# Kernel optimization log

Measured on AMD Instinct MI355X. Metric: run time of the kernel, lower is better.

## Reference

```python
import jax, jax.numpy as jnp
import numpy as np

B = 32; H = 56; W = 56; DIM = 384; HEADS = 12; WIN = 7; SHIFT = 3
HEAD_DIM = DIM // HEADS; SCALE = HEAD_DIM ** -0.5
N = WIN * WIN; NW = (H // WIN) * (W // WIN); L = H * W + 1; HID = 4 * DIM


def _rel_index():
    coords = np.stack(np.meshgrid(np.arange(WIN), np.arange(WIN), indexing='ij')).reshape(2, -1)
    rel = (coords[:, :, None] - coords[:, None, :]).transpose(1, 2, 0)
    rel[:, :, 0] += WIN - 1
    rel[:, :, 1] += WIN - 1
    rel[:, :, 0] *= 2 * WIN - 1
    return jnp.asarray(rel.sum(-1))  # (N, N) int


def _attn_mask():
    # standard Swin shift mask, padded with a zero column so the cls key is always visible
    img = np.zeros((H, W))
    sl = (slice(0, -WIN), slice(-WIN, -SHIFT), slice(-SHIFT, None))
    cnt = 0
    for hs in sl:
        for ws in sl:
            img[hs, ws] = cnt
            cnt += 1
    mw = img.reshape(H // WIN, WIN, W // WIN, WIN).transpose(0, 2, 1, 3).reshape(-1, N)
    m = mw[:, None, :] - mw[:, :, None]
    m = np.where(m != 0, -100.0, 0.0).astype(np.float32)
    m = np.pad(m, ((0, 0), (0, 0), (1, 0)))  # (nW, N, N+1)
    return jnp.asarray(m)


REL_INDEX = _rel_index()
ATTN_MASK = _attn_mask()


def _ln(x, g, b, eps=1e-5):
    m = x.mean(-1, keepdims=True)
    v = ((x - m) ** 2).mean(-1, keepdims=True)
    return (x - m) * jax.lax.rsqrt(v + eps) * g + b


def setup_inputs() -> dict:
    key = jax.random.key(0)
    ks = jax.random.split(key, 6)
    s = 0.02
    return dict(
        x=jax.random.normal(ks[0], (B, L, DIM), jnp.float32),
        norm1_g=jnp.ones((DIM,), jnp.float32), norm1_b=jnp.zeros((DIM,), jnp.float32),
        qkv_w=jax.random.normal(ks[1], (3 * DIM, DIM), jnp.float32) * s,
        qkv_b=jnp.zeros((3 * DIM,), jnp.float32),
        rel_bias_table=jax.random.normal(ks[2], ((2 * WIN - 1) ** 2, HEADS), jnp.float32) * s,
        proj_w=jax.random.normal(ks[3], (DIM, DIM), jnp.float32) * s,
        proj_b=jnp.zeros((DIM,), jnp.float32),
        norm2_g=jnp.ones((DIM,), jnp.float32), norm2_b=jnp.zeros((DIM,), jnp.float32),
        fc1_w=jax.random.normal(ks[4], (HID, DIM), jnp.float32) * s,
        fc1_b=jnp.zeros((HID,), jnp.float32),
        fc2_w=jax.random.normal(ks[5], (DIM, HID), jnp.float32) * s,
        fc2_b=jnp.zeros((DIM,), jnp.float32),
    )


def reference(x, norm1_g, norm1_b, qkv_w, qkv_b, rel_bias_table, proj_w, proj_b,
              norm2_g, norm2_b, fc1_w, fc1_b, fc2_w, fc2_b):
    Bx = x.shape[0]
    shortcut = x
    h = _ln(x, norm1_g, norm1_b)
    qkv = h @ qkv_w.T + qkv_b  # (B, L, 3C)

    # ---- global cls attention: token 0 attends to every token (ClsAttention) ----
    t = qkv.reshape(Bx, L, 3, HEADS, HEAD_DIM).transpose(2, 0, 3, 1, 4)  # (3, B, h, L, d)
    q0 = t[0, :, :, 0:1, :] * SCALE
    cls_attn = jax.nn.softmax(jnp.einsum('bhqd,bhkd->bhqk', q0, t[1]), axis=-1)
    cls_out = jnp.einsum('bhqk,bhkd->bhqd', cls_attn, t[2]).transpose(0, 2, 1, 3).reshape(Bx, 1, DIM)

    # ---- shifted-window attention for patch tokens, cls qkv prepended per window ----
    cls_qkv = qkv[:, :1]  # (B, 1, 3C)
    p = qkv[:, 1:].reshape(Bx, H, W, 3 * DIM)
    p = jnp.roll(p, (-SHIFT, -SHIFT), axis=(1, 2))
    pw = p.reshape(Bx, H // WIN, WIN, W // WIN, WIN, 3 * DIM).transpose(0, 1, 3, 2, 4, 5)
    pw = pw.reshape(Bx * NW, N, 3 * DIM)
    cls_rep = jnp.broadcast_to(cls_qkv[:, None], (Bx, NW, 1, 3 * DIM)).reshape(Bx * NW, 1, 3 * DIM)
    qkvw = jnp.concatenate([cls_rep, pw], axis=1)  # (B*nW, N+1, 3C)

    tw = qkvw.reshape(Bx * NW, N + 1, 3, HEADS, HEAD_DIM).transpose(2, 0, 3, 1, 4)
    q = tw[0, :, :, 1:, :] * SCALE  # patch queries (B*nW, h, N, d)
    attn = jnp.einsum('bhqd,bhkd->bhqk', q, tw[1])  # (B*nW, h, N, N+1)
    rel = rel_bias_table[REL_INDEX.reshape(-1)].reshape(N, N, HEADS).transpose(2, 0, 1)
    attn = jnp.concatenate([attn[..., :1], attn[..., 1:] + rel[None]], axis=-1)
    attn = attn.reshape(Bx, NW, HEADS, N, N + 1) + ATTN_MASK[None, :, None]
    attn = jax.nn.softmax(attn.reshape(Bx * NW, HEADS, N, N + 1), axis=-1)
    xw = jnp.einsum('bhqk,bhkd->bhqd', attn, tw[2]).transpose(0, 2, 1, 3).reshape(Bx * NW, N, DIM)

    # window reverse + reverse cyclic shift
    xp = xw.reshape(Bx, H // WIN, W // WIN, WIN, WIN, DIM).transpose(0, 1, 3, 2, 4, 5).reshape(Bx, H, W, DIM)
    xp = jnp.roll(xp, (SHIFT, SHIFT), axis=(1, 2)).reshape(Bx, H * W, DIM)

    a = jnp.concatenate([cls_out, xp], axis=1) @ proj_w.T + proj_b
    x1 = shortcut + a
    h2 = _ln(x1, norm2_g, norm2_b)
    h2 = jax.nn.gelu(h2 @ fc1_w.T + fc1_b, approximate=False)
    return x1 + (h2 @ fc2_w.T + fc2_b)
```

## Files before the change

### kernel.cpp

```cpp
#include <hip/hip_runtime.h>

#define DEVI __device__ __forceinline__

typedef __attribute__((ext_vector_type(8))) __bf16 bf16x8;
typedef __attribute__((ext_vector_type(4))) float f32x4;
typedef unsigned short u16;
typedef unsigned int u32;

static constexpr int kB = 32;
static constexpr int kL = 3137;
static constexpr int kM = kB * kL;
static constexpr int kHeads = 12;
static constexpr float kScale = 0.17677669529663687f;
static constexpr int kNC = 13;

DEVI u16 f2b(float f) {
  u32 u = __float_as_uint(f);
  u32 r = (u + 0x7fffu + ((u >> 16) & 1u)) >> 16;
  return (u16)r;
}
DEVI float blo(u32 u) { return __uint_as_float(u << 16); }
DEVI float bhi(u32 u) { return __uint_as_float(u & 0xffff0000u); }
DEVI float b2f(u16 h) { return __uint_as_float(((u32)h) << 16); }

DEVI void async16(const void* g, void* l) {
  __builtin_amdgcn_global_load_lds((const __attribute__((address_space(1))) u32*)g,
                                   (__attribute__((address_space(3))) u32*)l, 16, 0, 0);
}

DEVI float wred_max(float v) {
#pragma unroll
  for (int o = 32; o; o >>= 1) v = fmaxf(v, __shfl_xor(v, o));
  return v;
}
DEVI float wred_sum(float v) {
#pragma unroll
  for (int o = 32; o; o >>= 1) v += __shfl_xor(v, o);
  return v;
}

__global__ void cvt_bf16(const float* __restrict__ in, u16* __restrict__ out, int n) {
  int i = blockIdx.x * 256 + threadIdx.x;
  if (i < n) out[i] = f2b(in[i]);
}

__global__ __launch_bounds__(64)
void ln384(const float* __restrict__ x, const float* __restrict__ g,
           const float* __restrict__ b, u16* __restrict__ out, int rows) {
  int row = blockIdx.x;
  if (row >= rows) return;
  const float* xr = x + (size_t)row * 384;
  int t = threadIdx.x;
  float v[6], s = 0.f, s2 = 0.f;
#pragma unroll
  for (int i = 0; i < 6; i++) {
    v[i] = xr[t + 64 * i];
    s += v[i];
    s2 += v[i] * v[i];
  }
  s = wred_sum(s);
  s2 = wred_sum(s2);
  float mean = s * (1.f / 384.f);
  float var = s2 * (1.f / 384.f) - mean * mean;
  float rinv = rsqrtf(var + 1e-5f);
  u16* orow = out + (size_t)row * 384;
#pragma unroll
  for (int i = 0; i < 6; i++) {
    int c = t + 64 * i;
    orow[c] = f2b((v[i] - mean) * rinv * g[c] + b[c]);
  }
}

DEVI float gelu_exact(float v) { return 0.5f * v * (1.f + erff(v * 0.70710678118654752f)); }

template <int EPI>
__global__ __launch_bounds__(256)
void gemm_bt(const u16* __restrict__ A, const u16* __restrict__ W,
             const float* __restrict__ bias, const float* __restrict__ res,
             void* __restrict__ outp, int M, int N, int K, int NX) {
  {
  }
  const int nwg = gridDim.x;
  const int orig = blockIdx.x;
  const int xcd = orig & 7, rest = orig >> 3;
  const int q8 = nwg >> 3, r8 = nwg & 7;
  const int id = ((xcd < r8) ? xcd * (q8 + 1) : r8 * (q8 + 1) + (xcd - r8) * q8) + rest;
  const int col0 = (id % NX) * 128, row0 = (id / NX) * 128;

  const int tid = threadIdx.x, lane = tid & 63, wv = tid >> 6;
  __shared__ __align__(16) u16 As[3][128 * 32];
  __shared__ __align__(16) u16 Bs[3][128 * 32];
  f32x4 acc[4][4];
  f32x4 zero = {0.f, 0.f, 0.f, 0.f};
#pragma unroll
  for (int m = 0; m < 4; m++)
#pragma unroll
    for (int n = 0; n < 4; n++) acc[m][n] = zero;
  const int wm = wv >> 1, wn = wv & 1;
  const int c = lane & 15, g = lane >> 4;
  const int NT = K >> 5;

  auto stage = [&](int kt, int bfi) {
#pragma unroll
    for (int s = 0; s < 2; s++) {
      int ch = wv * 2 + s;
      int r = ch * 16 + (lane >> 2);
      int gnat = (lane & 3) ^ ((lane >> 3) & 3);
      int kk = kt * 32 + gnat * 8;
      const u16* gp = A + (size_t)min(row0 + r, M - 1) * K + kk;
      async16(gp, &As[bfi][ch * 512]);
      const u16* gq = W + (size_t)min(col0 + r, N - 1) * K + kk;
      async16(gq, &Bs[bfi][ch * 512]);
    }
  };

  stage(0, 0);
  stage(1, 1);
  int cur = 0;
  for (int kt = 0; kt < NT; ++kt) {
    if (kt + 1 < NT) asm volatile("s_waitcnt vmcnt(4)" ::: "memory");
    else             asm volatile("s_waitcnt vmcnt(0)" ::: "memory");
    __builtin_amdgcn_s_barrier();
    if (kt + 2 < NT) {
      int nb = cur + 2; if (nb >= 3) nb -= 3;
      stage(kt + 2, nb);
    }
    bf16x8 af[4], bw[4];
#pragma unroll
    for (int m = 0; m < 4; m++) {
      int row = wm * 64 + m * 16 + c;
      af[m] = *(const bf16x8*)&As[cur][row * 32 + ((g ^ ((row >> 1) & 3)) << 3)];
    }
#pragma unroll
    for (int n = 0; n < 4; n++) {
      int row = wn * 64 + n * 16 + c;
      bw[n] = *(const bf16x8*)&Bs[cur][row * 32 + ((g ^ ((row >> 1) & 3)) << 3)];
    }
    __builtin_amdgcn_s_setprio(1);
#pragma unroll
    for (int m = 0; m < 4; m++)
#pragma unroll
      for (int n = 0; n < 4; n++)
        acc[m][n] = __builtin_amdgcn_mfma_f32_16x16x32_bf16(af[m], bw[n], acc[m][n], 0, 0, 0);
    __builtin_amdgcn_s_setprio(0);
    cur = cur + 1; if (cur >= 3) cur -= 3;
  }

  int cc[4];
  float bv[4];
#pragma unroll
  for (int n = 0; n < 4; n++) {
    cc[n] = col0 + wn * 64 + n * 16 + c;
    bv[n] = bias[cc[n]];
  }
#pragma unroll
  for (int m = 0; m < 4; m++) {
    int rb = row0 + wm * 64 + m * 16 + (g << 2);
#pragma unroll
    for (int j = 0; j < 4; j++) {
      int r = rb + j;
      if (r < M) {
#pragma unroll
        for (int n = 0; n < 4; n++) {
          float vv = acc[m][n][j] + bv[n];
          size_t off = (size_t)r * N + cc[n];
          if constexpr (EPI == 0) {
            ((u16*)outp)[off] = f2b(vv);
          } else if constexpr (EPI == 1) {
            ((float*)outp)[off] = vv + res[off];
          } else {
            ((u16*)outp)[off] = f2b(gelu_exact(vv));
          }
        }
      }
    }
  }
}

__global__ __launch_bounds__(256)
void cls_part(const u16* __restrict__ qkv, float* __restrict__ parts) {
  int bh = blockIdx.x;
  int chunk = blockIdx.y;
  int b = bh / kHeads, h = bh % kHeads;
  __shared__ float qs[32];
  __shared__ float ps[256];
  __shared__ float red[8];
  __shared__ float part[8][32];
  int tid = threadIdx.x, lane = tid & 63, wv = tid >> 6;
  size_t rb = (size_t)b * kL;
  if (tid < 32) qs[tid] = b2f(qkv[rb * 1152 + h * 32 + tid]) * kScale;
  __syncthreads();
  int t0 = chunk * 256;
  int nTok = min(256, kL - t0);
  float s = -1e30f;
  if (tid < nTok) {
    const u16* kp = qkv + (rb + t0 + tid) * 1152 + 384 + h * 32;
    s = 0.f;
#pragma unroll
    for (int g4 = 0; g4 < 4; g4++) {
      uint4 u = *(const uint4*)(kp + g4 * 8);
      s += qs[g4*8+0]*blo(u.x) + qs[g4*8+1]*bhi(u.x)
         + qs[g4*8+2]*blo(u.y) + qs[g4*8+3]*bhi(u.y)
         + qs[g4*8+4]*blo(u.z) + qs[g4*8+5]*bhi(u.z)
         + qs[g4*8+6]*blo(u.w) + qs[g4*8+7]*bhi(u.w);
    }
  }
  float m = wred_max(s);
  if (lane == 0) red[wv] = m;
  __syncthreads();
  float gm = fmaxf(fmaxf(red[0], red[1]), fmaxf(red[2], red[3]));
  float p = (tid < nTok) ? __expf(s - gm) : 0.f;
  ps[tid] = p;
  float ls = wred_sum(p);
  if (lane == 0) red[4 + wv] = ls;
  __syncthreads();
  float tot = red[4] + red[5] + red[6] + red[7];
  int d = tid & 31, g = tid >> 5;
  float a = 0.f;
  for (int t = g; t < nTok; t += 8)
    a += ps[t] * b2f(qkv[(rb + t0 + t) * 1152 + 768 + h * 32 + d]);
  part[g][d] = a;
  __syncthreads();
  if (tid < 32) {
    float o = 0.f;
#pragma unroll
    for (int g2 = 0; g2 < 8; g2++) o += part[g2][tid];
    float* pp = parts + ((size_t)bh * kNC + chunk) * 34;
    pp[2 + tid] = o;
    if (tid == 0) { pp[0] = gm; pp[1] = tot; }
  }
}

__global__ __launch_bounds__(64)
void cls_reduce(const float* __restrict__ parts, u16* __restrict__ aout) {
  int bh = blockIdx.x;
  int b = bh / kHeads, h = bh % kHeads;
  int tid = threadIdx.x;
  __shared__ float sm[kNC], ss[kNC];
  if (tid < kNC) {
    sm[tid] = parts[((size_t)bh * kNC + tid) * 34];
    ss[tid] = parts[((size_t)bh * kNC + tid) * 34 + 1];
  }
  __syncthreads();
  float M = -1e30f;
#pragma unroll
  for (int c = 0; c < kNC; c++) M = fmaxf(M, sm[c]);
  float W = 0.f;
#pragma unroll
  for (int c = 0; c < kNC; c++) W += ss[c] * __expf(sm[c] - M);
  if (tid < 32) {
    float o = 0.f;
#pragma unroll
    for (int c = 0; c < kNC; c++)
      o += parts[((size_t)bh * kNC + c) * 34 + 2 + tid] * __expf(sm[c] - M);
    aout[(size_t)b * kL * 384 + h * 32 + tid] = f2b(o / W);
  }
}

__global__ __launch_bounds__(256)
void bias_pre(const float* __restrict__ relb, float* __restrict__ bf) {
  int blk = blockIdx.x;
  int cls = blk / 12, h = blk % 12;
  int clsH = (cls >> 1) & 1, clsW = cls & 1;
  for (int idx = threadIdx.x; idx < 4096; idx += 256) {
    int k = idx >> 6, q = idx & 63;
    float v = 0.f;
    if (k >= 50) {
      v = -1e9f;
    } else if (k >= 1 && q < 49) {
      int kt = k - 1, ki = kt / 7, kj = kt % 7;
      int qi = q / 7, qj = q % 7;
      v = relb[((qi - ki + 6) * 13 + (qj - kj + 6)) * 12 + h];
      int rq = (clsH ? (qi < 4 ? 1 : 2) : 0) * 3 + (clsW ? (qj < 4 ? 1 : 2) : 0);
      int rk = (clsH ? (ki < 4 ? 1 : 2) : 0) * 3 + (clsW ? (kj < 4 ? 1 : 2) : 0);
      if (rq != rk) v -= 100.f;
    }
    bf[(size_t)blk * 4096 + idx] = v;
  }
}

__global__ __launch_bounds__(256)
void win_attn2(const u16* __restrict__ qkv, const float* __restrict__ biasf,
               u16* __restrict__ aout) {
  const int tid = threadIdx.x, lane = tid & 63, wv = tid >> 6;
  const int gid = blockIdx.x * 4 + wv;
  const int h = gid % 12;
  const int wr = gid / 12;
  const int win = wr & 63, b = wr >> 6;
  const int wi = win >> 3, wj = win & 7;
  const int cls = ((wi == 7) ? 2 : 0) + ((wj == 7) ? 1 : 0);
  const int c = lane & 15, g = lane >> 4;

  __shared__ __align__(16) u16 KS[4][64 * 40];
  __shared__ __align__(16) u16 VT[4][32 * 72];
  __shared__ int RW[4][52];
  u16* Ks = KS[wv];
  u16* Vt = VT[wv];
  int* Rows = RW[wv];

#pragma unroll
  for (int it = 0; it < 2; ++it) {
    int idx = it * 64 + lane;
    int tok = idx >> 1, half = idx & 1;
    if (tok < 50) {
      int row;
      if (tok == 0) {
        row = b * kL;
      } else {
        int n = tok - 1;
        int i = n / 7, j = n % 7;
        int r = wi * 7 + i, c2 = wj * 7 + j;
        int orr = r + 3; if (orr >= 56) orr -= 56;
        int occ = c2 + 3; if (occ >= 56) occ -= 56;
        row = b * kL + 1 + orr * 56 + occ;
      }
      if (half == 0) Rows[tok] = row;
      const u16* base = qkv + (size_t)row * 1152 + h * 32 + half * 16;
      uint4 k0 = *(const uint4*)(base + 384);
      uint4 k1 = *(const uint4*)(base + 384 + 8);
      *(uint4*)&Ks[tok * 40 + half * 16] = k0;
      *(uint4*)&Ks[tok * 40 + half * 16 + 8] = k1;
      uint4 v0 = *(const uint4*)(base + 768);
      uint4 v1 = *(const uint4*)(base + 768 + 8);
      u32 vw[8] = {v0.x, v0.y, v0.z, v0.w, v1.x, v1.y, v1.z, v1.w};
#pragma unroll
      for (int m = 0; m < 8; ++m) {
        Vt[(half * 16 + m * 2 + 0) * 72 + tok] = (u16)(vw[m] & 0xffffu);
        Vt[(half * 16 + m * 2 + 1) * 72 + tok] = (u16)(vw[m] >> 16);
      }
    } else {
      uint4 z = {0u, 0u, 0u, 0u};
      *(uint4*)&Ks[tok * 40 + half * 16] = z;
      *(uint4*)&Ks[tok * 40 + half * 16 + 8] = z;
#pragma unroll
      for (int m = 0; m < 16; ++m) Vt[(half * 16 + m) * 72 + tok] = 0;
    }
  }
  __syncthreads();

  bf16x8 qf[4];
#pragma unroll
  for (int nt = 0; nt < 4; ++nt) {
    int q = nt * 16 + c;
    if (q > 48) q = 48;
    const u16* qp = qkv + (size_t)Rows[q + 1] * 1152 + h * 32 + g * 8;
    qf[nt] = *(const bf16x8*)qp;
  }

  f32x4 s[4][4];
  {
    f32x4 z = {0.f, 0.f, 0.f, 0.f};
    bf16x8 kf[4];
#pragma unroll
    for (int mt = 0; mt < 4; ++mt)
      kf[mt] = *(const bf16x8*)&Ks[(mt * 16 + c) * 40 + g * 8];
#pragma unroll
    for (int mt = 0; mt < 4; ++mt)
#pragma unroll
      for (int nt = 0; nt < 4; ++nt)
        s[mt][nt] = __builtin_amdgcn_mfma_f32_16x16x32_bf16(kf[mt], qf[nt], z, 0, 0, 0);
  }

  const float* bp = biasf + (size_t)(cls * 12 + h) * 4096;
  u32 wq[4][8];
#pragma unroll
  for (int nt = 0; nt < 4; ++nt) {
    float pv[16];
#pragma unroll
    for (int mt = 0; mt < 4; ++mt)
#pragma unroll
      for (int r = 0; r < 4; ++r)
        pv[mt * 4 + r] = s[mt][nt][r] * kScale + bp[(mt * 16 + g * 4 + r) * 64 + nt * 16 + c];
    float mx = pv[0];
#pragma unroll
    for (int i2 = 1; i2 < 16; ++i2) mx = fmaxf(mx, pv[i2]);
    mx = fmaxf(mx, __shfl_xor(mx, 16));
    mx = fmaxf(mx, __shfl_xor(mx, 32));
    float sum = 0.f;
#pragma unroll
    for (int i2 = 0; i2 < 16; ++i2) { pv[i2] = __expf(pv[i2] - mx); sum += pv[i2]; }
    sum += __shfl_xor(sum, 16);
    sum += __shfl_xor(sum, 32);
    float rs = 1.f / sum;
#pragma unroll
    for (int i2 = 0; i2 < 16; ++i2) pv[i2] *= rs;
#pragma unroll
    for (int mt = 0; mt < 4; ++mt) {
      u32 w0, w1;
      asm("v_cvt_pk_bf16_f32 %0, %1, %2" : "=v"(w0) : "v"(pv[mt * 4 + 0]), "v"(pv[mt * 4 + 1]));
      asm("v_cvt_pk_bf16_f32 %0, %1, %2" : "=v"(w1) : "v"(pv[mt * 4 + 2]), "v"(pv[mt * 4 + 3]));
      wq[nt][mt * 2 + 0] = w0;
      wq[nt][mt * 2 + 1] = w1;
    }
  }

  bf16x8 pa[4][2];
#pragma unroll
  for (int mt2 = 0; mt2 < 4; ++mt2)
#pragma unroll
    for (int ks = 0; ks < 2; ++ks) {
      union { u32 u[4]; bf16x8 v; } cvt;
#pragma unroll
      for (int wj2 = 0; wj2 < 4; ++wj2) {
        int srcLane = c + 16 * (((g & 1) << 1) + (wj2 >> 1));
        u32 a0 = (u32)__shfl((int)wq[mt2][(2 * ks + 0) * 2 + (wj2 & 1)], srcLane);
        u32 a1 = (u32)__shfl((int)wq[mt2][(2 * ks + 1) * 2 + (wj2 & 1)], srcLane);
        cvt.u[wj2] = (g < 2) ? a0 : a1;
      }
      pa[mt2][ks] = cvt.v;
    }

  f32x4 o[4][2];
  f32x4 z2 = {0.f, 0.f, 0.f, 0.f};
#pragma unroll
  for (int mt2 = 0; mt2 < 4; ++mt2)
#pragma unroll
    for (int ntd = 0; ntd < 2; ++ntd) o[mt2][ntd] = z2;
#pragma unroll
  for (int ks = 0; ks < 2; ++ks) {
    bf16x8 vf[2];
#pragma unroll
    for (int ntd = 0; ntd < 2; ++ntd)
      vf[ntd] = *(const bf16x8*)&Vt[(ntd * 16 + c) * 72 + ks * 32 + g * 8];
#pragma unroll
    for (int mt2 = 0; mt2 < 4; ++mt2)
#pragma unroll
      for (int ntd = 0; ntd < 2; ++ntd)
        o[mt2][ntd] = __builtin_amdgcn_mfma_f32_16x16x32_bf16(pa[mt2][ks], vf[ntd], o[mt2][ntd], 0, 0, 0);
  }

#pragma unroll
  for (int mt2 = 0; mt2 < 4; ++mt2)
#pragma unroll
    for (int r = 0; r < 4; ++r) {
      int q = mt2 * 16 + g * 4 + r;
      if (q < 49) {
        int row = Rows[q + 1];
        u16* op = aout + (size_t)row * 384 + h * 32 + c;
        op[0]  = f2b(o[mt2][0][r]);
        op[16] = f2b(o[mt2][1][r]);
      }
    }
}

extern "C" void kernel_launch(void* const* d_in, const int* in_sizes, int n_in,
                              void* d_out, int out_size, void* d_ws, size_t ws_size,
                              hipStream_t stream) {
  const float* x      = (const float*)d_in[0];
  const float* n1g    = (const float*)d_in[1];
  const float* n1b    = (const float*)d_in[2];
  const float* qkv_w  = (const float*)d_in[3];
  const float* qkv_b  = (const float*)d_in[4];
  const float* relb   = (const float*)d_in[5];
  const float* proj_w = (const float*)d_in[6];
  const float* proj_b = (const float*)d_in[7];
  const float* n2g    = (const float*)d_in[8];
  const float* n2b    = (const float*)d_in[9];
  const float* fc1_w  = (const float*)d_in[10];
  const float* fc1_b  = (const float*)d_in[11];
  const float* fc2_w  = (const float*)d_in[12];
  const float* fc2_b  = (const float*)d_in[13];
  float* out = (float*)d_out;
  char* ws = (char*)d_ws;

  u16* wqkv  = (u16*)(ws + 0);
  float* biasf = (float*)(ws + 0);
  u16* wproj = (u16*)(ws + 884736);
  u16* wfc1  = (u16*)(ws + 1179648);
  u16* wfc2  = (u16*)(ws + 2359296);
  u16* qkvb  = (u16*)(ws + 3538944);
  u16* h2b   = (u16*)(ws + 3538944);
  u16* gb    = (u16*)(ws + 3538944 + 41943040);
  u16* hbuf  = (u16*)(ws + 234823680);
  float* parts = (float*)d_out;

  cvt_bf16<<<dim3((442368 + 255) / 256), 256, 0, stream>>>(qkv_w, wqkv, 442368);
  cvt_bf16<<<dim3((147456 + 255) / 256), 256, 0, stream>>>(proj_w, wproj, 147456);
  cvt_bf16<<<dim3((589824 + 255) / 256), 256, 0, stream>>>(fc1_w, wfc1, 589824);
  cvt_bf16<<<dim3((589824 + 255) / 256), 256, 0, stream>>>(fc2_w, wfc2, 589824);

  ln384<<<kM, 64, 0, stream>>>(x, n1g, n1b, hbuf, kM);
  gemm_bt<0><<<9 * 785, 256, 0, stream>>>(hbuf, wqkv, qkv_b, nullptr, qkvb, kM, 1152, 384, 9);
  bias_pre<<<48, 256, 0, stream>>>(relb, biasf);
  cls_part<<<dim3(kB * kHeads, kNC), 256, 0, stream>>>(qkvb, parts);
  cls_reduce<<<kB * kHeads, 64, 0, stream>>>(parts, hbuf);
  win_attn2<<<kB * 64 * kHeads / 4, 256, 0, stream>>>(qkvb, biasf, hbuf);
  gemm_bt<1><<<3 * 785, 256, 0, stream>>>(hbuf, wproj, proj_b, x, out, kM, 384, 384, 3);

  for (int c = 0; c < 2; c++) {
    int r0 = c * 50192, nr = 50192;
    ln384<<<nr, 64, 0, stream>>>(out + (size_t)r0 * 384, n2g, n2b, h2b, nr);
    gemm_bt<2><<<12 * 393, 256, 0, stream>>>(h2b, wfc1, fc1_b, nullptr, gb, nr, 1536, 384, 12);
    gemm_bt<1><<<3 * 393, 256, 0, stream>>>(gb, wfc2, fc2_b, out + (size_t)r0 * 384,
                                            out + (size_t)r0 * 384, nr, 384, 1536, 3);
  }
}
```

Measured before the change: 1.000 ms.

## Restructure GEMM staging into half-tile double buffers and vectorize layernorm

The GEMM's three-stage 32-wide K ring is replaced by a double-buffered 64-wide K tile split into two 32-wide halves. Global base pointers and the swizzle offset are precomputed once, and the loop is unrolled by 4 to cut address arithmetic and index bookkeeping in the main loop. Layernorm now packs four rows per 256-thread block and uses float2 loads and packed bf16x2 stores, which cuts the block count and widens memory transactions. The new swizzle pattern changes LDS bank mapping, so it risks new conflicts if it was derived incorrectly.

```diff
diff --git a/kernel.cpp b/kernel.cpp
--- a/kernel.cpp
+++ b/kernel.cpp
@@ -44,30 +44,36 @@
   if (i < n) out[i] = f2b(in[i]);
 }
 
-__global__ __launch_bounds__(64)
-void ln384(const float* __restrict__ x, const float* __restrict__ g,
-           const float* __restrict__ b, u16* __restrict__ out, int rows) {
-  int row = blockIdx.x;
+__global__ __launch_bounds__(256)
+void ln384(const float* __restrict__ x, const float* __restrict__ gam,
+           const float* __restrict__ bet, u16* __restrict__ out, int rows) {
+  int row = blockIdx.x * 4 + (threadIdx.x >> 6);
   if (row >= rows) return;
-  const float* xr = x + (size_t)row * 384;
-  int t = threadIdx.x;
-  float v[6], s = 0.f, s2 = 0.f;
-#pragma unroll
-  for (int i = 0; i < 6; i++) {
-    v[i] = xr[t + 64 * i];
-    s += v[i];
-    s2 += v[i] * v[i];
+  int lane = threadIdx.x & 63;
+  const float2* xr = (const float2*)(x + (size_t)row * 384);
+  float2 v[3];
+  float s = 0.f, s2 = 0.f;
+#pragma unroll
+  for (int i = 0; i < 3; i++) {
+    v[i] = xr[lane + 64 * i];
+    s += v[i].x + v[i].y;
+    s2 += v[i].x * v[i].x + v[i].y * v[i].y;
   }
   s = wred_sum(s);
   s2 = wred_sum(s2);
   float mean = s * (1.f / 384.f);
   float var = s2 * (1.f / 384.f) - mean * mean;
   float rinv = rsqrtf(var + 1e-5f);
-  u16* orow = out + (size_t)row * 384;
-#pragma unroll
-  for (int i = 0; i < 6; i++) {
-    int c = t + 64 * i;
-    orow[c] = f2b((v[i] - mean) * rinv * g[c] + b[c]);
+  const float2* gp = (const float2*)gam;
+  const float2* bp = (const float2*)bet;
+  u32* orow = (u32*)(out + (size_t)row * 384);
+#pragma unroll
+  for (int i = 0; i < 3; i++) {
+    int idx = lane + 64 * i;
+    float2 gg = gp[idx], bb = bp[idx];
+    float lo = (v[i].x - mean) * rinv * gg.x + bb.x;
+    float hi = (v[i].y - mean) * rinv * gg.y + bb.y;
+    orow[idx] = (u32)f2b(lo) | ((u32)f2b(hi) << 16);
   }
 }
 
@@ -78,8 +84,6 @@
 void gemm_bt(const u16* __restrict__ A, const u16* __restrict__ W,
              const float* __restrict__ bias, const float* __restrict__ res,
              void* __restrict__ outp, int M, int N, int K, int NX) {
-  {
-  }
   const int nwg = gridDim.x;
   const int orig = blockIdx.x;
   const int xcd = orig & 7, rest = orig >> 3;
@@ -88,54 +92,62 @@
   const int col0 = (id % NX) * 128, row0 = (id / NX) * 128;
 
   const int tid = threadIdx.x, lane = tid & 63, wv = tid >> 6;
-  __shared__ __align__(16) u16 As[3][128 * 32];
-  __shared__ __align__(16) u16 Bs[3][128 * 32];
+  const int c = lane & 15, g = lane >> 4;
+  const int wm = wv >> 1, wn = wv & 1;
+
+  __shared__ __align__(16) u16 Ah[2][2][4096];
+  __shared__ __align__(16) u16 Bh[2][2][4096];
+
   f32x4 acc[4][4];
   f32x4 zero = {0.f, 0.f, 0.f, 0.f};
 #pragma unroll
   for (int m = 0; m < 4; m++)
 #pragma unroll
     for (int n = 0; n < 4; n++) acc[m][n] = zero;
-  const int wm = wv >> 1, wn = wv & 1;
-  const int c = lane & 15, g = lane >> 4;
-  const int NT = K >> 5;
-
-  auto stage = [&](int kt, int bfi) {
-#pragma unroll
-    for (int s = 0; s < 2; s++) {
-      int ch = wv * 2 + s;
-      int r = ch * 16 + (lane >> 2);
-      int gnat = (lane & 3) ^ ((lane >> 3) & 3);
-      int kk = kt * 32 + gnat * 8;
-      const u16* gp = A + (size_t)min(row0 + r, M - 1) * K + kk;
-      async16(gp, &As[bfi][ch * 512]);
-      const u16* gq = W + (size_t)min(col0 + r, N - 1) * K + kk;
-      async16(gq, &Bs[bfi][ch * 512]);
+
+  const int rsub = wv * 16 + (lane >> 2);
+  const int gsrc = (lane & 3) ^ ((rsub ^ (rsub >> 2)) & 3);
+  const u16* baseA[2];
+  const u16* baseB[2];
+#pragma unroll
+  for (int i = 0; i < 2; i++) {
+    baseA[i] = A + (size_t)min(row0 + i * 64 + rsub, M - 1) * K + gsrc * 8;
+    baseB[i] = W + (size_t)min(col0 + i * 64 + rsub, N - 1) * K + gsrc * 8;
+  }
+
+  auto stage = [&](int kt, int h, int d) {
+    int off = kt * 64 + h * 32;
+#pragma unroll
+    for (int i = 0; i < 2; i++) {
+      async16(baseA[i] + off, &Ah[d][h][i * 2048 + wv * 512]);
+      async16(baseB[i] + off, &Bh[d][h][i * 2048 + wv * 512]);
     }
   };
 
-  stage(0, 0);
-  stage(1, 1);
-  int cur = 0;
-  for (int kt = 0; kt < NT; ++kt) {
-    if (kt + 1 < NT) asm volatile("s_waitcnt vmcnt(4)" ::: "memory");
-    else             asm volatile("s_waitcnt vmcnt(0)" ::: "memory");
+  const int axor = ((g ^ ((c ^ (c >> 2)) & 3)) << 3);
+
+  const int NPH = K >> 5;
+  stage(0, 0, 0);
+  stage(0, 1, 0);
+
+#pragma unroll 4
+  for (int ph = 0; ph < NPH; ++ph) {
+    const int kt = ph >> 1, h = ph & 1, d = kt & 1;
+    if (ph + 1 < NPH) asm volatile("s_waitcnt vmcnt(4)" ::: "memory");
+    else              asm volatile("s_waitcnt vmcnt(0)" ::: "memory");
     __builtin_amdgcn_s_barrier();
-    if (kt + 2 < NT) {
-      int nb = cur + 2; if (nb >= 3) nb -= 3;
-      stage(kt + 2, nb);
-    }
+    int ph2 = ph + 2;
+    if (ph2 < NPH) stage(ph2 >> 1, ph2 & 1, (ph2 >> 1) & 1);
+
+    const u16* As_ = Ah[d][h];
+    const u16* Bs_ = Bh[d][h];
     bf16x8 af[4], bw[4];
 #pragma unroll
-    for (int m = 0; m < 4; m++) {
-      int row = wm * 64 + m * 16 + c;
-      af[m] = *(const bf16x8*)&As[cur][row * 32 + ((g ^ ((row >> 1) & 3)) << 3)];
-    }
-#pragma unroll
-    for (int n = 0; n < 4; n++) {
-      int row = wn * 64 + n * 16 + c;
-      bw[n] = *(const bf16x8*)&Bs[cur][row * 32 + ((g ^ ((row >> 1) & 3)) << 3)];
-    }
+    for (int m = 0; m < 4; m++)
+      af[m] = *(const bf16x8*)&As_[(wm * 64 + m * 16 + c) * 32 + axor];
+#pragma unroll
+    for (int n = 0; n < 4; n++)
+      bw[n] = *(const bf16x8*)&Bs_[(wn * 64 + n * 16 + c) * 32 + axor];
     __builtin_amdgcn_s_setprio(1);
 #pragma unroll
     for (int m = 0; m < 4; m++)
@@ -143,7 +155,6 @@
       for (int n = 0; n < 4; n++)
         acc[m][n] = __builtin_amdgcn_mfma_f32_16x16x32_bf16(af[m], bw[n], acc[m][n], 0, 0, 0);
     __builtin_amdgcn_s_setprio(0);
-    cur = cur + 1; if (cur >= 3) cur -= 3;
   }
 
   int cc[4];
@@ -479,7 +490,7 @@
   cvt_bf16<<<dim3((589824 + 255) / 256), 256, 0, stream>>>(fc1_w, wfc1, 589824);
   cvt_bf16<<<dim3((589824 + 255) / 256), 256, 0, stream>>>(fc2_w, wfc2, 589824);
 
-  ln384<<<kM, 64, 0, stream>>>(x, n1g, n1b, hbuf, kM);
+  ln384<<<(kM + 3) / 4, 256, 0, stream>>>(x, n1g, n1b, hbuf, kM);
   gemm_bt<0><<<9 * 785, 256, 0, stream>>>(hbuf, wqkv, qkv_b, nullptr, qkvb, kM, 1152, 384, 9);
   bias_pre<<<48, 256, 0, stream>>>(relb, biasf);
   cls_part<<<dim3(kB * kHeads, kNC), 256, 0, stream>>>(qkvb, parts);
@@ -489,7 +500,7 @@
 
   for (int c = 0; c < 2; c++) {
     int r0 = c * 50192, nr = 50192;
-    ln384<<<nr, 64, 0, stream>>>(out + (size_t)r0 * 384, n2g, n2b, h2b, nr);
+    ln384<<<(nr + 3) / 4, 256, 0, stream>>>(out + (size_t)r0 * 384, n2g, n2b, h2b, nr);
     gemm_bt<2><<<12 * 393, 256, 0, stream>>>(h2b, wfc1, fc1_b, nullptr, gb, nr, 1536, 384, 12);
     gemm_bt<1><<<3 * 393, 256, 0, stream>>>(gb, wfc2, fc2_b, out + (size_t)r0 * 384,
                                             out + (size_t)r0 * 384, nr, 384, 1536, 3);
```

Result: slower. 1.181 ms (+18.1%).
